# Kernel optimization log

Measured on AMD Instinct MI355X. Metric: run time of the kernel, lower is better.

The kernel has to match this reference:

```python
import jax, jax.numpy as jnp
import numpy as np

NEG_SLOPE = 0.2  # PyG GATConv default negative_slope


def gat_conv(x, src, dst, W, a_src, a_dst, b, n_nodes, concat):
    # x: [N, F_in]; W: [F_in, H*C]; a_src/a_dst: [H, C]; b: [H*C] or [C]
    H, C = a_src.shape
    h = (x @ W).reshape(n_nodes, H, C)                      # [N, H, C]
    al_src = jnp.sum(h * a_src[None], axis=-1)              # [N, H]
    al_dst = jnp.sum(h * a_dst[None], axis=-1)              # [N, H]
    e = jax.nn.leaky_relu(al_src[src] + al_dst[dst], NEG_SLOPE)  # [E, H]
    # segment softmax over incoming edges of each destination node
    m = jax.ops.segment_max(e, dst, num_segments=n_nodes)  # [N, H]
    ex = jnp.exp(e - m[dst])                                # [E, H]
    s = jax.ops.segment_sum(ex, dst, num_segments=n_nodes)  # [N, H]
    alpha = ex / s[dst]                                     # [E, H]
    msg = h[src] * alpha[:, :, None]                        # [E, H, C]
    out = jax.ops.segment_sum(msg, dst, num_segments=n_nodes)  # [N, H, C]
    if concat:
        out = out.reshape(n_nodes, H * C)
    else:
        out = out.mean(axis=1)
    return out + b


def setup_inputs() -> dict:
    key = jax.random.key(0)
    ks = jax.random.split(key, 10)
    N, E = 100000, 800000
    F_in, C1, H, C2 = 128, 32, 8, 16
    x = jax.random.normal(ks[0], (N, F_in), dtype=jnp.float32)
    edge_index = jax.random.randint(ks[1], (2, E), 0, N, dtype=jnp.int64)
    s = 0.05
    return {
        "x": x,
        "edge_index": edge_index,
        "W1": jax.random.normal(ks[2], (F_in, H * C1), dtype=jnp.float32) * s,
        "att_src1": jax.random.normal(ks[3], (H, C1), dtype=jnp.float32) * s,
        "att_dst1": jax.random.normal(ks[4], (H, C1), dtype=jnp.float32) * s,
        "b1": jnp.zeros((H * C1,), dtype=jnp.float32),
        "W2": jax.random.normal(ks[5], (H * C1, H * C2), dtype=jnp.float32) * s,
        "att_src2": jax.random.normal(ks[6], (H, C2), dtype=jnp.float32) * s,
        "att_dst2": jax.random.normal(ks[7], (H, C2), dtype=jnp.float32) * s,
        "b2": jnp.zeros((C2,), dtype=jnp.float32),
    }


def reference(x, edge_index, W1, att_src1, att_dst1, b1, W2, att_src2, att_dst2, b2):
    n = x.shape[0]
    # PyG GATConv default add_self_loops=True (same augmented edge set for both layers)
    loops = jnp.arange(n, dtype=edge_index.dtype)
    src = jnp.concatenate([edge_index[0], loops])
    dst = jnp.concatenate([edge_index[1], loops])
    # dropout_p = 0.0 -> dropout is identity (eval-mode math)
    h = gat_conv(x, src, dst, W1, att_src1, att_dst1, b1, n, concat=True)
    h = jax.nn.elu(h)
    out = gat_conv(h, src, dst, W2, att_src2, att_dst2, b2, n, concat=False)
    return jax.nn.log_softmax(out, axis=-1)
```

## Files before the change

### kernel.cpp

```cpp
#include <hip/hip_runtime.h>
#include <cstdint>
#include <cstddef>


typedef short bf16x8 __attribute__((ext_vector_type(8)));
typedef unsigned short u16x8 __attribute__((ext_vector_type(8)));
typedef float f32x4 __attribute__((ext_vector_type(4)));

__device__ inline unsigned short f2bf(float f) {
  unsigned u = __float_as_uint(f);
  unsigned r = (u + 0x7FFFu + ((u >> 16) & 1u)) >> 16;
  return (unsigned short)r;
}
__device__ inline float bf2f(unsigned short s) {
  return __uint_as_float((unsigned)s << 16);
}

__device__ inline unsigned char fp8enc(float x) {
  unsigned u = __float_as_uint(x);
  unsigned s = u >> 31;
  float ax = fminf(fabsf(x), 448.f);
  unsigned em;
  if (ax >= 0.015625f) {
    unsigned b = __float_as_uint(ax);
    unsigned b2 = b + 0x7FFFFu + ((b >> 20) & 1u);
    em = (b2 >> 20) - 960u;
    if (em > 126u) em = 126u;
  } else {
    em = (unsigned)__float2int_rn(ax * 512.f);
  }
  return (unsigned char)((s << 7) | em);
}
__device__ inline float fp8dec_sw(unsigned b8) {
  unsigned s = b8 >> 7, em = b8 & 0x7Fu;
  float fn = __uint_as_float((s << 31) | ((em + 960u) << 20));
  float fd = (float)em * 0.001953125f;
  fd = s ? -fd : fd;
  return em >= 8u ? fn : fd;
}
__device__ inline void fp8dec4(unsigned w, float* out) {
#if __has_builtin(__builtin_amdgcn_cvt_f32_fp8)
  out[0] = __builtin_amdgcn_cvt_f32_fp8(w, 0);
  out[1] = __builtin_amdgcn_cvt_f32_fp8(w, 1);
  out[2] = __builtin_amdgcn_cvt_f32_fp8(w, 2);
  out[3] = __builtin_amdgcn_cvt_f32_fp8(w, 3);
#else
  out[0] = fp8dec_sw(w & 0xFFu);
  out[1] = fp8dec_sw((w >> 8) & 0xFFu);
  out[2] = fp8dec_sw((w >> 16) & 0xFFu);
  out[3] = fp8dec_sw((w >> 24) & 0xFFu);
#endif
}


__global__ __launch_bounds__(256) void detect_kernel(const int* __restrict__ words,
                                                     int E, int* __restrict__ flag) {
  int t = threadIdx.x;
  int n = E < 1024 ? E : 1024;
  int cnt = 0;
  for (int i = t; i < n; i += 256) cnt += (words[2 * i + 1] != 0) ? 1 : 0;
  for (int m = 1; m < 64; m <<= 1) cnt += __shfl_xor(cnt, m);
  if ((t & 63) == 0 && cnt) atomicAdd(flag, cnt);
}

__global__ __launch_bounds__(256) void extract_kernel(const void* __restrict__ ei,
                                                      int E, int N,
                                                      const int* __restrict__ flag,
                                                      int* __restrict__ src,
                                                      int* __restrict__ dst,
                                                      int* __restrict__ deg) {
  int e = blockIdx.x * 256 + threadIdx.x;
  int ET = E + N;
  if (e >= ET) return;
  int s, d;
  if (e < E) {
    if (flag[0] == 0) {
      const long long* p = (const long long*)ei;
      s = (int)p[e];
      d = (int)p[(size_t)E + e];
    } else {
      const int* p = (const int*)ei;
      s = p[e];
      d = p[E + e];
    }
  } else {
    s = d = e - E;
  }
  src[e] = s;
  dst[e] = d;
  atomicAdd(&deg[d], 1);
}

__global__ __launch_bounds__(256) void scan_a(const int* __restrict__ deg,
                                              int* __restrict__ off,
                                              int* __restrict__ bsum, int N) {
  __shared__ int sh[256];
  int b = blockIdx.x, t = threadIdx.x;
  int base = b * 2048 + t * 8;
  int p[8];
  int run = 0;
#pragma unroll
  for (int j = 0; j < 8; ++j) {
    int v = (base + j < N) ? deg[base + j] : 0;
    run += v;
    p[j] = run;
  }
  sh[t] = run;
  __syncthreads();
  for (int d = 1; d < 256; d <<= 1) {
    int x = (t >= d) ? sh[t - d] : 0;
    __syncthreads();
    if (t >= d) sh[t] += x;
    __syncthreads();
  }
  int excl = sh[t] - run;
#pragma unroll
  for (int j = 0; j < 8; ++j)
    if (base + j < N) off[base + j + 1] = excl + p[j];
  if (t == 255) bsum[b] = sh[255];
}

__global__ void scan_b(int* __restrict__ bsum, int nb) {
  int t = threadIdx.x;
  int orig = (t < nb) ? bsum[t] : 0;
  int v = orig;
  for (int d = 1; d < 64; d <<= 1) {
    int u = __shfl_up(v, d);
    if (t >= d) v += u;
  }
  if (t < nb) bsum[t] = v - orig;
}

__global__ __launch_bounds__(256) void scan_c(int* __restrict__ off,
                                              const int* __restrict__ bsum, int N) {
  int i = blockIdx.x * 256 + threadIdx.x;
  if (i == 0) off[0] = 0;
  if (i >= 1 && i <= N) off[i] += bsum[(i - 1) / 2048];
}

__global__ __launch_bounds__(256) void fill_kernel(const int* __restrict__ src,
                                                   const int* __restrict__ dst,
                                                   const int* __restrict__ off,
                                                   int* __restrict__ deg,
                                                   int* __restrict__ csr, int ET) {
  int e = blockIdx.x * 256 + threadIdx.x;
  if (e >= ET) return;
  int d = dst[e];
  int p = atomicSub(&deg[d], 1) - 1;
  csr[off[d] + p] = src[e];
}

__global__ __launch_bounds__(256) void pack_kernel(const float* __restrict__ W,
                                                   short* __restrict__ Wp,
                                                   int NOUT, int total) {
  int NT = NOUT >> 4;
  for (int idx = blockIdx.x * 256 + threadIdx.x; idx < total;
       idx += gridDim.x * 256) {
    int j = idx & 7;
    int lane = (idx >> 3) & 63;
    int st = idx >> 9;
    int s = st / NT, t = st - s * NT;
    int k = s * 32 + (lane >> 4) * 8 + j;
    int n = t * 16 + (lane & 15);
    Wp[idx] = (short)f2bf(W[(size_t)k * NOUT + n]);
  }
}

template <int K, int NOUT, bool AF32, bool OUT_FP8>
__global__ __launch_bounds__(256) void mfma_gemm(const void* __restrict__ Av,
                                                 const short* __restrict__ Bp,
                                                 short* __restrict__ Cb,
                                                 unsigned char* __restrict__ Cq,
                                                 const float* __restrict__ as,
                                                 const float* __restrict__ ad,
                                                 float* __restrict__ alsO,
                                                 float* __restrict__ aldO, int M) {
  constexpr int KS = K / 32;
  constexpr int NT = NOUT / 16;
  constexpr int RST = NOUT + 8;
  constexpr int QST = NOUT + 16;
  constexpr int C = NOUT / 8;
  __shared__ __align__(16) short lds[64 * RST];
  __shared__ __align__(16) unsigned char ldsq[OUT_FP8 ? 64 * QST : 16];
  const int tid = threadIdx.x;
  const int wave = tid >> 6, lane = tid & 63;
  const int lo = lane & 15, hi = lane >> 4;
  const int rowA = blockIdx.x * 64 + wave * 16 + lo;
  const bool inb = rowA < M;

  f32x4 acc[NT];
#pragma unroll
  for (int t = 0; t < NT; ++t) acc[t] = (f32x4){0.f, 0.f, 0.f, 0.f};

#pragma unroll
  for (int s = 0; s < KS; ++s) {
    bf16x8 af;
    if constexpr (AF32) {
      const float* Ap = (const float*)Av;
      float v[8];
      if (inb) {
        const float4 x0 = *(const float4*)&Ap[(size_t)rowA * K + s * 32 + hi * 8];
        const float4 x1 = *(const float4*)&Ap[(size_t)rowA * K + s * 32 + hi * 8 + 4];
        v[0] = x0.x; v[1] = x0.y; v[2] = x0.z; v[3] = x0.w;
        v[4] = x1.x; v[5] = x1.y; v[6] = x1.z; v[7] = x1.w;
      } else {
#pragma unroll
        for (int j = 0; j < 8; ++j) v[j] = 0.f;
      }
#pragma unroll
      for (int j = 0; j < 8; ++j) af[j] = (short)f2bf(v[j]);
    } else {
      const short* Ab = (const short*)Av;
      if (inb) {
        af = *(const bf16x8*)&Ab[(size_t)rowA * K + s * 32 + hi * 8];
      } else {
#pragma unroll
        for (int j = 0; j < 8; ++j) af[j] = 0;
      }
    }
#pragma unroll
    for (int t = 0; t < NT; ++t) {
      bf16x8 bf = *(const bf16x8*)&Bp[((size_t)(s * NT + t) * 64 + lane) * 8];
      acc[t] = __builtin_amdgcn_mfma_f32_16x16x32_bf16(af, bf, acc[t], 0, 0, 0);
    }
  }

#pragma unroll
  for (int t = 0; t < NT; ++t)
#pragma unroll
    for (int r = 0; r < 4; ++r) {
      int row = wave * 16 + hi * 4 + r;
      lds[row * RST + t * 16 + lo] = (short)f2bf(acc[t][r]);
      if constexpr (OUT_FP8)
        ldsq[row * QST + t * 16 + lo] = fp8enc(acc[t][r]);
    }
  __syncthreads();

  if constexpr (OUT_FP8) {
#pragma unroll
    for (int i = 0; i < (64 * NOUT / 16) / 256; ++i) {
      int v = i * 256 + tid;
      int r = v >> 4;
      int c = v & 15;
      int grow = blockIdx.x * 64 + r;
      if (grow < M)
        *(float4*)&Cq[(size_t)grow * NOUT + c * 16] =
            *(const float4*)&ldsq[r * QST + c * 16];
    }
  } else {
    constexpr int VECS = 64 * NOUT / 8;
#pragma unroll
    for (int i = 0; i < VECS / 256; ++i) {
      int v = i * 256 + tid;
      int r = v / (NOUT / 8);
      int c = v % (NOUT / 8);
      int grow = blockIdx.x * 64 + r;
      if (grow < M)
        *(float4*)&Cb[(size_t)grow * NOUT + c * 8] =
            *(const float4*)&lds[r * RST + c * 8];
    }
  }

  constexpr int SEGS = NOUT / 64;
  if (tid < 64 * SEGS) {
    int r = tid / SEGS, seg = tid % SEGS;
    int grow = blockIdx.x * 64 + r;
    float ps[8], pd[8];
#pragma unroll
    for (int k = 0; k < 8; ++k) { ps[k] = 0.f; pd[k] = 0.f; }
#pragma unroll
    for (int k = 0; k < 8; ++k) {
      int b = seg + SEGS * k;
      u16x8 u = *(const u16x8*)&lds[r * RST + b * 8];
#pragma unroll
      for (int j = 0; j < 8; ++j) {
        float hv = bf2f(u[j]);
        ps[k] = fmaf(hv, as[k * C + seg * 8 + j], ps[k]);
        pd[k] = fmaf(hv, ad[k * C + seg * 8 + j], pd[k]);
      }
    }
#pragma unroll
    for (int d = 1; d < SEGS; d <<= 1)
#pragma unroll
      for (int k = 0; k < 8; ++k) {
        ps[k] += __shfl_xor(ps[k], d);
        pd[k] += __shfl_xor(pd[k], d);
      }
    if (seg == 0 && grow < M) {
      *(float4*)&alsO[(size_t)grow * 8] = make_float4(ps[0], ps[1], ps[2], ps[3]);
      *(float4*)&alsO[(size_t)grow * 8 + 4] = make_float4(ps[4], ps[5], ps[6], ps[7]);
      *(float4*)&aldO[(size_t)grow * 8] = make_float4(pd[0], pd[1], pd[2], pd[3]);
      *(float4*)&aldO[(size_t)grow * 8 + 4] = make_float4(pd[4], pd[5], pd[6], pd[7]);
    }
  }
}

__global__ __launch_bounds__(256) void agg1_kernel(const unsigned char* __restrict__ hq,
                                                   const float* __restrict__ als,
                                                   const float* __restrict__ ald,
                                                   const int* __restrict__ off,
                                                   const int* __restrict__ csr,
                                                   const float* __restrict__ bias,
                                                   short* __restrict__ outb, int N) {
  int wid = blockIdx.x * 4 + (threadIdx.x >> 6);
  if (wid >= N) return;
  int lane = threadIdx.x & 63;
  int rs = off[wid], re = off[wid + 1];
  int es = lane >> 5;
  int gl = lane & 31;
  int head = gl >> 2;
  float aldv = ald[wid * 8 + head];

  float acc[8];
#pragma unroll
  for (int j = 0; j < 8; ++j) acc[j] = 0.f;
  float ws = 0.f;

  int i = rs + es;
  for (; i + 2 < re; i += 4) {
    int s0 = csr[i], s1 = csr[i + 2];
    float e0 = als[s0 * 8 + head] + aldv;
    float e1 = als[s1 * 8 + head] + aldv;
    uint2 u0 = *(const uint2*)&hq[(size_t)s0 * 256 + gl * 8];
    uint2 u1 = *(const uint2*)&hq[(size_t)s1 * 256 + gl * 8];
    e0 = e0 > 0.f ? e0 : 0.2f * e0;
    e1 = e1 > 0.f ? e1 : 0.2f * e1;
    float w0 = __expf(e0), w1 = __expf(e1);
    ws += w0 + w1;
    float d0a[4], d0b[4], d1a[4], d1b[4];
    fp8dec4(u0.x, d0a); fp8dec4(u0.y, d0b);
    fp8dec4(u1.x, d1a); fp8dec4(u1.y, d1b);
#pragma unroll
    for (int j = 0; j < 4; ++j) {
      acc[j] = fmaf(w0, d0a[j], acc[j]);
      acc[j + 4] = fmaf(w0, d0b[j], acc[j + 4]);
      acc[j] = fmaf(w1, d1a[j], acc[j]);
      acc[j + 4] = fmaf(w1, d1b[j], acc[j + 4]);
    }
  }
  if (i < re) {
    int s0 = csr[i];
    float e0 = als[s0 * 8 + head] + aldv;
    uint2 u0 = *(const uint2*)&hq[(size_t)s0 * 256 + gl * 8];
    e0 = e0 > 0.f ? e0 : 0.2f * e0;
    float w0 = __expf(e0);
    ws += w0;
    float d0a[4], d0b[4];
    fp8dec4(u0.x, d0a); fp8dec4(u0.y, d0b);
#pragma unroll
    for (int j = 0; j < 4; ++j) {
      acc[j] = fmaf(w0, d0a[j], acc[j]);
      acc[j + 4] = fmaf(w0, d0b[j], acc[j + 4]);
    }
  }

  ws += __shfl_xor(ws, 32);
#pragma unroll
  for (int j = 0; j < 8; ++j) acc[j] += __shfl_xor(acc[j], 32);
  float inv = 1.f / ws;

  if (lane < 32) {
    u16x8 o;
#pragma unroll
    for (int j = 0; j < 8; ++j) {
      float v = acc[j] * inv + bias[gl * 8 + j];
      o[j] = f2bf(v > 0.f ? v : expm1f(v));
    }
    *(u16x8*)&outb[(size_t)wid * 256 + gl * 8] = o;
  }
}

__global__ __launch_bounds__(256) void agg2_kernel(const short* __restrict__ hb,
                                                   const float* __restrict__ als,
                                                   const float* __restrict__ ald,
                                                   const int* __restrict__ off,
                                                   const int* __restrict__ csr,
                                                   const float* __restrict__ bias,
                                                   float* __restrict__ out, int N) {
  constexpr int LPG = 16;
  constexpr int NS = 4;
  int wid = blockIdx.x * 4 + (threadIdx.x >> 6);
  if (wid >= N) return;
  int lane = threadIdx.x & 63;
  int rs = off[wid], re = off[wid + 1];
  int es = lane / LPG;
  int gl = lane & (LPG - 1);
  int head = gl >> 1;
  float aldv = ald[wid * 8 + head];

  float acc[8];
#pragma unroll
  for (int j = 0; j < 8; ++j) acc[j] = 0.f;
  float ws = 0.f;

  int i = rs + es;
  for (; i + NS < re; i += 2 * NS) {
    int s0 = csr[i], s1 = csr[i + NS];
    float e0 = als[s0 * 8 + head] + aldv;
    float e1 = als[s1 * 8 + head] + aldv;
    u16x8 u0 = *(const u16x8*)&hb[(size_t)s0 * 128 + gl * 8];
    u16x8 u1 = *(const u16x8*)&hb[(size_t)s1 * 128 + gl * 8];
    e0 = e0 > 0.f ? e0 : 0.2f * e0;
    e1 = e1 > 0.f ? e1 : 0.2f * e1;
    float w0 = __expf(e0), w1 = __expf(e1);
    ws += w0 + w1;
#pragma unroll
    for (int j = 0; j < 8; ++j)
      acc[j] = fmaf(w1, bf2f(u1[j]), fmaf(w0, bf2f(u0[j]), acc[j]));
  }
  if (i < re) {
    int s0 = csr[i];
    float e0 = als[s0 * 8 + head] + aldv;
    u16x8 u0 = *(const u16x8*)&hb[(size_t)s0 * 128 + gl * 8];
    e0 = e0 > 0.f ? e0 : 0.2f * e0;
    float w0 = __expf(e0);
    ws += w0;
#pragma unroll
    for (int j = 0; j < 8; ++j) acc[j] = fmaf(w0, bf2f(u0[j]), acc[j]);
  }

#pragma unroll
  for (int d = LPG; d < 64; d <<= 1) {
    ws += __shfl_xor(ws, d);
#pragma unroll
    for (int j = 0; j < 8; ++j) acc[j] += __shfl_xor(acc[j], d);
  }
  float inv = 1.f / ws;

#pragma unroll
  for (int j = 0; j < 8; ++j) acc[j] *= inv;
#pragma unroll
  for (int d = 2; d <= 8; d <<= 1)
#pragma unroll
    for (int j = 0; j < 8; ++j) acc[j] += __shfl_xor(acc[j], d);
  int p = gl & 1;
  float v[8];
#pragma unroll
  for (int j = 0; j < 8; ++j) v[j] = acc[j] * 0.125f + bias[p * 8 + j];
  float m = v[0];
#pragma unroll
  for (int j = 1; j < 8; ++j) m = fmaxf(m, v[j]);
  m = fmaxf(m, __shfl_xor(m, 1));
  float se = 0.f;
#pragma unroll
  for (int j = 0; j < 8; ++j) se += __expf(v[j] - m);
  se += __shfl_xor(se, 1);
  float lse = m + logf(se);
  if (lane < 2) {
    *(float4*)&out[(size_t)wid * 16 + p * 8] =
        make_float4(v[0] - lse, v[1] - lse, v[2] - lse, v[3] - lse);
    *(float4*)&out[(size_t)wid * 16 + p * 8 + 4] =
        make_float4(v[4] - lse, v[5] - lse, v[6] - lse, v[7] - lse);
  }
}


extern "C" void kernel_launch(void* const* d_in, const int* in_sizes, int n_in,
                              void* d_out, int out_size, void* d_ws, size_t ws_size,
                              hipStream_t stream) {
  const float* x = (const float*)d_in[0];
  const void* ei = d_in[1];
  const float* W1 = (const float*)d_in[2];
  const float* as1 = (const float*)d_in[3];
  const float* ad1 = (const float*)d_in[4];
  const float* b1 = (const float*)d_in[5];
  const float* W2 = (const float*)d_in[6];
  const float* as2 = (const float*)d_in[7];
  const float* ad2 = (const float*)d_in[8];
  const float* b2 = (const float*)d_in[9];
  float* out = (float*)d_out;

  const int N = out_size / 16;
  const int E = in_sizes[1] / 2;
  const int ET = E + N;

  char* p = (char*)d_ws;
  auto alloc = [&](size_t bytes) {
    char* r = p;
    p += (bytes + 255) & ~(size_t)255;
    return (void*)r;
  };
  unsigned char* h1q = (unsigned char*)alloc((size_t)N * 256);
  short* hactb = (short*)alloc((size_t)N * 256 * 2);
  short* h2b = (short*)alloc((size_t)N * 128 * 2);
  float* als = (float*)alloc((size_t)N * 8 * 4);
  float* ald = (float*)alloc((size_t)N * 8 * 4);
  int* src32 = (int*)alloc((size_t)ET * 4);
  int* dst32 = (int*)alloc((size_t)ET * 4);
  int* csr = (int*)alloc((size_t)ET * 4);
  int* deg = (int*)alloc((size_t)N * 4);
  int* off = (int*)alloc((size_t)(N + 1) * 4);
  int* bsum = (int*)alloc(256 * 4);
  int* flag = (int*)alloc(256);
  short* W1p = (short*)alloc(128 * 256 * 2);
  short* W2p = (short*)alloc(256 * 128 * 2);

  hipMemsetAsync(deg, 0, (size_t)N * 4, stream);
  hipMemsetAsync(flag, 0, 4, stream);

  detect_kernel<<<1, 256, 0, stream>>>((const int*)ei, E, flag);
  int gridET = (ET + 255) / 256;
  extract_kernel<<<gridET, 256, 0, stream>>>(ei, E, N, flag, src32, dst32, deg);
  int nscan = (N + 2047) / 2048;
  scan_a<<<nscan, 256, 0, stream>>>(deg, off, bsum, N);
  scan_b<<<1, 64, 0, stream>>>(bsum, nscan);
  scan_c<<<(N + 256) / 256, 256, 0, stream>>>(off, bsum, N);
  fill_kernel<<<gridET, 256, 0, stream>>>(src32, dst32, off, deg, csr, ET);

  pack_kernel<<<128, 256, 0, stream>>>(W1, W1p, 256, 128 * 256);
  pack_kernel<<<128, 256, 0, stream>>>(W2, W2p, 128, 256 * 128);

  int gemmGrid = (N + 63) / 64;
  int nodeGrid = (N + 3) / 4;

  mfma_gemm<128, 256, true, true><<<gemmGrid, 256, 0, stream>>>(
      x, W1p, nullptr, h1q, as1, ad1, als, ald, N);
  agg1_kernel<<<nodeGrid, 256, 0, stream>>>(h1q, als, ald, off, csr, b1, hactb, N);
  mfma_gemm<256, 128, false, false><<<gemmGrid, 256, 0, stream>>>(
      hactb, W2p, h2b, nullptr, as2, ad2, als, ald, N);
  agg2_kernel<<<nodeGrid, 256, 0, stream>>>(h2b, als, ald, off, csr, b2, out, N);
}
```

Measured before the change: 338.5 us.

## Fuse edge extraction into layer-1 GEMM, merge scans/packs, use FP8 for layer-2 features

Edge extraction and degree counting are merged into the layer-1 GEMM launch as extra blocks, the two weight-pack kernels become one, and scan_b is folded into scan_c. The two memsets become one. Layer-2 features are now stored as FP8 (reusing the h1q buffer) instead of bf16, halving gather bytes in agg2. Leaky ReLU uses fmaxf. The aim is fewer launches and less memory traffic, at the cost of FP8 precision loss in the second layer and a larger LDS footprint for the second GEMM.

```diff
diff --git a/kernel.cpp b/kernel.cpp
--- a/kernel.cpp
+++ b/kernel.cpp
@@ -63,34 +63,6 @@
   if ((t & 63) == 0 && cnt) atomicAdd(flag, cnt);
 }
 
-__global__ __launch_bounds__(256) void extract_kernel(const void* __restrict__ ei,
-                                                      int E, int N,
-                                                      const int* __restrict__ flag,
-                                                      int* __restrict__ src,
-                                                      int* __restrict__ dst,
-                                                      int* __restrict__ deg) {
-  int e = blockIdx.x * 256 + threadIdx.x;
-  int ET = E + N;
-  if (e >= ET) return;
-  int s, d;
-  if (e < E) {
-    if (flag[0] == 0) {
-      const long long* p = (const long long*)ei;
-      s = (int)p[e];
-      d = (int)p[(size_t)E + e];
-    } else {
-      const int* p = (const int*)ei;
-      s = p[e];
-      d = p[E + e];
-    }
-  } else {
-    s = d = e - E;
-  }
-  src[e] = s;
-  dst[e] = d;
-  atomicAdd(&deg[d], 1);
-}
-
 __global__ __launch_bounds__(256) void scan_a(const int* __restrict__ deg,
                                               int* __restrict__ off,
                                               int* __restrict__ bsum, int N) {
@@ -120,22 +92,27 @@
   if (t == 255) bsum[b] = sh[255];
 }
 
-__global__ void scan_b(int* __restrict__ bsum, int nb) {
+__global__ __launch_bounds__(256) void scan_c(int* __restrict__ off,
+                                              const int* __restrict__ bsum,
+                                              int N, int nb) {
+  __shared__ int sb[64];
   int t = threadIdx.x;
-  int orig = (t < nb) ? bsum[t] : 0;
-  int v = orig;
-  for (int d = 1; d < 64; d <<= 1) {
-    int u = __shfl_up(v, d);
-    if (t >= d) v += u;
-  }
-  if (t < nb) bsum[t] = v - orig;
-}
-
-__global__ __launch_bounds__(256) void scan_c(int* __restrict__ off,
-                                              const int* __restrict__ bsum, int N) {
-  int i = blockIdx.x * 256 + threadIdx.x;
+  if (t < 64) {
+    int v = (t < nb) ? bsum[t] : 0;
+    for (int d = 1; d < 64; d <<= 1) {
+      int u = __shfl_up(v, d);
+      if (t >= d) v += u;
+    }
+    sb[t] = v;
+  }
+  __syncthreads();
+  int i = blockIdx.x * 256 + t;
   if (i == 0) off[0] = 0;
-  if (i >= 1 && i <= N) off[i] += bsum[(i - 1) / 2048];
+  if (i >= 1 && i <= N) {
+    int c = (i - 1) / 2048;
+    int excl = (c == 0) ? 0 : sb[c - 1];
+    off[i] += excl;
+  }
 }
 
 __global__ __launch_bounds__(256) void fill_kernel(const int* __restrict__ src,
@@ -150,42 +127,46 @@
   csr[off[d] + p] = src[e];
 }
 
-__global__ __launch_bounds__(256) void pack_kernel(const float* __restrict__ W,
-                                                   short* __restrict__ Wp,
-                                                   int NOUT, int total) {
+__device__ inline void pack_one(const float* __restrict__ W,
+                                short* __restrict__ Wp, int NOUT, int idx) {
   int NT = NOUT >> 4;
-  for (int idx = blockIdx.x * 256 + threadIdx.x; idx < total;
-       idx += gridDim.x * 256) {
-    int j = idx & 7;
-    int lane = (idx >> 3) & 63;
-    int st = idx >> 9;
-    int s = st / NT, t = st - s * NT;
-    int k = s * 32 + (lane >> 4) * 8 + j;
-    int n = t * 16 + (lane & 15);
-    Wp[idx] = (short)f2bf(W[(size_t)k * NOUT + n]);
-  }
-}
-
-template <int K, int NOUT, bool AF32, bool OUT_FP8>
-__global__ __launch_bounds__(256) void mfma_gemm(const void* __restrict__ Av,
-                                                 const short* __restrict__ Bp,
-                                                 short* __restrict__ Cb,
-                                                 unsigned char* __restrict__ Cq,
-                                                 const float* __restrict__ as,
-                                                 const float* __restrict__ ad,
-                                                 float* __restrict__ alsO,
-                                                 float* __restrict__ aldO, int M) {
+  int j = idx & 7;
+  int lane = (idx >> 3) & 63;
+  int st = idx >> 9;
+  int s = st / NT, t = st - s * NT;
+  int k = s * 32 + (lane >> 4) * 8 + j;
+  int n = t * 16 + (lane & 15);
+  Wp[idx] = (short)f2bf(W[(size_t)k * NOUT + n]);
+}
+
+__global__ __launch_bounds__(256) void pack2_kernel(const float* __restrict__ W1,
+                                                    short* __restrict__ W1p,
+                                                    const float* __restrict__ W2,
+                                                    short* __restrict__ W2p) {
+  int b = blockIdx.x, t = threadIdx.x;
+  if (b < 128) pack_one(W1, W1p, 256, b * 256 + t);
+  else         pack_one(W2, W2p, 128, (b - 128) * 256 + t);
+}
+
+template <int K, int NOUT, bool AF32>
+__device__ void gemm_body(int bx, const void* __restrict__ Av,
+                          const short* __restrict__ Bp,
+                          unsigned char* __restrict__ Cq,
+                          const float* __restrict__ as,
+                          const float* __restrict__ ad,
+                          float* __restrict__ alsO,
+                          float* __restrict__ aldO, int M) {
   constexpr int KS = K / 32;
   constexpr int NT = NOUT / 16;
   constexpr int RST = NOUT + 8;
   constexpr int QST = NOUT + 16;
   constexpr int C = NOUT / 8;
   __shared__ __align__(16) short lds[64 * RST];
-  __shared__ __align__(16) unsigned char ldsq[OUT_FP8 ? 64 * QST : 16];
+  __shared__ __align__(16) unsigned char ldsq[64 * QST];
   const int tid = threadIdx.x;
   const int wave = tid >> 6, lane = tid & 63;
   const int lo = lane & 15, hi = lane >> 4;
-  const int rowA = blockIdx.x * 64 + wave * 16 + lo;
+  const int rowA = bx * 64 + wave * 16 + lo;
   const bool inb = rowA < M;
 
   f32x4 acc[NT];
@@ -231,40 +212,26 @@
     for (int r = 0; r < 4; ++r) {
       int row = wave * 16 + hi * 4 + r;
       lds[row * RST + t * 16 + lo] = (short)f2bf(acc[t][r]);
-      if constexpr (OUT_FP8)
-        ldsq[row * QST + t * 16 + lo] = fp8enc(acc[t][r]);
+      ldsq[row * QST + t * 16 + lo] = fp8enc(acc[t][r]);
     }
   __syncthreads();
 
-  if constexpr (OUT_FP8) {
-#pragma unroll
-    for (int i = 0; i < (64 * NOUT / 16) / 256; ++i) {
-      int v = i * 256 + tid;
-      int r = v >> 4;
-      int c = v & 15;
-      int grow = blockIdx.x * 64 + r;
-      if (grow < M)
-        *(float4*)&Cq[(size_t)grow * NOUT + c * 16] =
-            *(const float4*)&ldsq[r * QST + c * 16];
-    }
-  } else {
-    constexpr int VECS = 64 * NOUT / 8;
-#pragma unroll
-    for (int i = 0; i < VECS / 256; ++i) {
-      int v = i * 256 + tid;
-      int r = v / (NOUT / 8);
-      int c = v % (NOUT / 8);
-      int grow = blockIdx.x * 64 + r;
-      if (grow < M)
-        *(float4*)&Cb[(size_t)grow * NOUT + c * 8] =
-            *(const float4*)&lds[r * RST + c * 8];
-    }
+  constexpr int CPR = NOUT / 16;
+#pragma unroll
+  for (int i = 0; i < (64 * CPR) / 256; ++i) {
+    int v = i * 256 + tid;
+    int r = v / CPR;
+    int c = v % CPR;
+    int grow = bx * 64 + r;
+    if (grow < M)
+      *(float4*)&Cq[(size_t)grow * NOUT + c * 16] =
+          *(const float4*)&ldsq[r * QST + c * 16];
   }
 
   constexpr int SEGS = NOUT / 64;
   if (tid < 64 * SEGS) {
     int r = tid / SEGS, seg = tid % SEGS;
-    int grow = blockIdx.x * 64 + r;
+    int grow = bx * 64 + r;
     float ps[8], pd[8];
 #pragma unroll
     for (int k = 0; k < 8; ++k) { ps[k] = 0.f; pd[k] = 0.f; }
@@ -293,6 +260,51 @@
       *(float4*)&aldO[(size_t)grow * 8 + 4] = make_float4(pd[4], pd[5], pd[6], pd[7]);
     }
   }
+}
+
+__global__ __launch_bounds__(256) void mega1_kernel(
+    const float* __restrict__ x, const short* __restrict__ W1p,
+    unsigned char* __restrict__ h1q, const float* __restrict__ as1,
+    const float* __restrict__ ad1, float* __restrict__ als,
+    float* __restrict__ ald, int M, int gemmGrid,
+    const void* __restrict__ ei, int E, int N, const int* __restrict__ flag,
+    int* __restrict__ src, int* __restrict__ dst, int* __restrict__ deg) {
+  int bx = blockIdx.x;
+  if (bx < gemmGrid) {
+    gemm_body<128, 256, true>(bx, x, W1p, h1q, as1, ad1, als, ald, M);
+  } else {
+    int e = (bx - gemmGrid) * 256 + threadIdx.x;
+    int ET = E + N;
+    if (e >= ET) return;
+    int s, d;
+    if (e < E) {
+      if (flag[0] == 0) {
+        const long long* p = (const long long*)ei;
+        s = (int)p[e];
+        d = (int)p[(size_t)E + e];
+      } else {
+        const int* p = (const int*)ei;
+        s = p[e];
+        d = p[E + e];
+      }
+    } else {
+      s = d = e - E;
+    }
+    src[e] = s;
+    dst[e] = d;
+    atomicAdd(&deg[d], 1);
+  }
+}
+
+template <int K, int NOUT, bool AF32>
+__global__ __launch_bounds__(256) void mfma_gemm(const void* __restrict__ Av,
+                                                 const short* __restrict__ Bp,
+                                                 unsigned char* __restrict__ Cq,
+                                                 const float* __restrict__ as,
+                                                 const float* __restrict__ ad,
+                                                 float* __restrict__ alsO,
+                                                 float* __restrict__ aldO, int M) {
+  gemm_body<K, NOUT, AF32>(blockIdx.x, Av, Bp, Cq, as, ad, alsO, aldO, M);
 }
 
 __global__ __launch_bounds__(256) void agg1_kernel(const unsigned char* __restrict__ hq,
@@ -323,8 +335,8 @@
     float e1 = als[s1 * 8 + head] + aldv;
     uint2 u0 = *(const uint2*)&hq[(size_t)s0 * 256 + gl * 8];
     uint2 u1 = *(const uint2*)&hq[(size_t)s1 * 256 + gl * 8];
-    e0 = e0 > 0.f ? e0 : 0.2f * e0;
-    e1 = e1 > 0.f ? e1 : 0.2f * e1;
+    e0 = fmaxf(e0, 0.2f * e0);
+    e1 = fmaxf(e1, 0.2f * e1);
     float w0 = __expf(e0), w1 = __expf(e1);
     ws += w0 + w1;
     float d0a[4], d0b[4], d1a[4], d1b[4];
@@ -342,7 +354,7 @@
     int s0 = csr[i];
     float e0 = als[s0 * 8 + head] + aldv;
     uint2 u0 = *(const uint2*)&hq[(size_t)s0 * 256 + gl * 8];
-    e0 = e0 > 0.f ? e0 : 0.2f * e0;
+    e0 = fmaxf(e0, 0.2f * e0);
     float w0 = __expf(e0);
     ws += w0;
     float d0a[4], d0b[4];
@@ -370,21 +382,19 @@
   }
 }
 
-__global__ __launch_bounds__(256) void agg2_kernel(const short* __restrict__ hb,
+__global__ __launch_bounds__(256) void agg2_kernel(const unsigned char* __restrict__ hq,
                                                    const float* __restrict__ als,
                                                    const float* __restrict__ ald,
                                                    const int* __restrict__ off,
                                                    const int* __restrict__ csr,
                                                    const float* __restrict__ bias,
                                                    float* __restrict__ out, int N) {
-  constexpr int LPG = 16;
-  constexpr int NS = 4;
   int wid = blockIdx.x * 4 + (threadIdx.x >> 6);
   if (wid >= N) return;
   int lane = threadIdx.x & 63;
   int rs = off[wid], re = off[wid + 1];
-  int es = lane / LPG;
-  int gl = lane & (LPG - 1);
+  int es = lane >> 4;
+  int gl = lane & 15;
   int head = gl >> 1;
   float aldv = ald[wid * 8 + head];
 
@@ -394,33 +404,38 @@
   float ws = 0.f;
 
   int i = rs + es;
-  for (; i + NS < re; i += 2 * NS) {
-    int s0 = csr[i], s1 = csr[i + NS];
+  for (; i + 4 < re; i += 8) {
+    int s0 = csr[i], s1 = csr[i + 4];
     float e0 = als[s0 * 8 + head] + aldv;
     float e1 = als[s1 * 8 + head] + aldv;
-    u16x8 u0 = *(const u16x8*)&hb[(size_t)s0 * 128 + gl * 8];
-    u16x8 u1 = *(const u16x8*)&hb[(size_t)s1 * 128 + gl * 8];
-    e0 = e0 > 0.f ? e0 : 0.2f * e0;
-    e1 = e1 > 0.f ? e1 : 0.2f * e1;
+    uint2 u0 = *(const uint2*)&hq[(size_t)s0 * 128 + gl * 8];
+    uint2 u1 = *(const uint2*)&hq[(size_t)s1 * 128 + gl * 8];
+    e0 = fmaxf(e0, 0.2f * e0);
+    e1 = fmaxf(e1, 0.2f * e1);
     float w0 = __expf(e0), w1 = __expf(e1);
     ws += w0 + w1;
+    float d0[8], d1[8];
+    fp8dec4(u0.x, d0); fp8dec4(u0.y, d0 + 4);
+    fp8dec4(u1.x, d1); fp8dec4(u1.y, d1 + 4);
 #pragma unroll
     for (int j = 0; j < 8; ++j)
-      acc[j] = fmaf(w1, bf2f(u1[j]), fmaf(w0, bf2f(u0[j]), acc[j]));
+      acc[j] = fmaf(w1, d1[j], fmaf(w0, d0[j], acc[j]));
   }
   if (i < re) {
     int s0 = csr[i];
     float e0 = als[s0 * 8 + head] + aldv;
-    u16x8 u0 = *(const u16x8*)&hb[(size_t)s0 * 128 + gl * 8];
-    e0 = e0 > 0.f ? e0 : 0.2f * e0;
+    uint2 u0 = *(const uint2*)&hq[(size_t)s0 * 128 + gl * 8];
+    e0 = fmaxf(e0, 0.2f * e0);
     float w0 = __expf(e0);
     ws += w0;
-#pragma unroll
-    for (int j = 0; j < 8; ++j) acc[j] = fmaf(w0, bf2f(u0[j]), acc[j]);
-  }
-
-#pragma unroll
-  for (int d = LPG; d < 64; d <<= 1) {
+    float d0[8];
+    fp8dec4(u0.x, d0); fp8dec4(u0.y, d0 + 4);
+#pragma unroll
+    for (int j = 0; j < 8; ++j) acc[j] = fmaf(w0, d0[j], acc[j]);
+  }
+
+#pragma unroll
+  for (int d = 16; d < 64; d <<= 1) {
     ws += __shfl_xor(ws, d);
 #pragma unroll
     for (int j = 0; j < 8; ++j) acc[j] += __shfl_xor(acc[j], d);
@@ -482,41 +497,38 @@
   };
   unsigned char* h1q = (unsigned char*)alloc((size_t)N * 256);
   short* hactb = (short*)alloc((size_t)N * 256 * 2);
-  short* h2b = (short*)alloc((size_t)N * 128 * 2);
   float* als = (float*)alloc((size_t)N * 8 * 4);
   float* ald = (float*)alloc((size_t)N * 8 * 4);
   int* src32 = (int*)alloc((size_t)ET * 4);
   int* dst32 = (int*)alloc((size_t)ET * 4);
   int* csr = (int*)alloc((size_t)ET * 4);
   int* deg = (int*)alloc((size_t)N * 4);
+  int* flag = (int*)alloc(256);
   int* off = (int*)alloc((size_t)(N + 1) * 4);
   int* bsum = (int*)alloc(256 * 4);
-  int* flag = (int*)alloc(256);
   short* W1p = (short*)alloc(128 * 256 * 2);
   short* W2p = (short*)alloc(256 * 128 * 2);
-
-  hipMemsetAsync(deg, 0, (size_t)N * 4, stream);
-  hipMemsetAsync(flag, 0, 4, stream);
+  unsigned char* h2q = h1q;
+
+  hipMemsetAsync(deg, 0, (((size_t)N * 4 + 255) & ~(size_t)255) + 4, stream);
 
   detect_kernel<<<1, 256, 0, stream>>>((const int*)ei, E, flag);
+  pack2_kernel<<<256, 256, 0, stream>>>(W1, W1p, W2, W2p);
+
+  int gemmGrid = (N + 63) / 64;
   int gridET = (ET + 255) / 256;
-  extract_kernel<<<gridET, 256, 0, stream>>>(ei, E, N, flag, src32, dst32, deg);
+  int nodeGrid = (N + 3) / 4;
   int nscan = (N + 2047) / 2048;
+
+  mega1_kernel<<<gemmGrid + gridET, 256, 0, stream>>>(
+      x, W1p, h1q, as1, ad1, als, ald, N, gemmGrid, ei, E, N, flag, src32,
+      dst32, deg);
   scan_a<<<nscan, 256, 0, stream>>>(deg, off, bsum, N);
-  scan_b<<<1, 64, 0, stream>>>(bsum, nscan);
-  scan_c<<<(N + 256) / 256, 256, 0, stream>>>(off, bsum, N);
+  scan_c<<<(N + 256) / 256, 256, 0, stream>>>(off, bsum, N, nscan);
   fill_kernel<<<gridET, 256, 0, stream>>>(src32, dst32, off, deg, csr, ET);
 
-  pack_kernel<<<128, 256, 0, stream>>>(W1, W1p, 256, 128 * 256);
-  pack_kernel<<<128, 256, 0, stream>>>(W2, W2p, 128, 256 * 128);
-
-  int gemmGrid = (N + 63) / 64;
-  int nodeGrid = (N + 3) / 4;
-
-  mfma_gemm<128, 256, true, true><<<gemmGrid, 256, 0, stream>>>(
-      x, W1p, nullptr, h1q, as1, ad1, als, ald, N);
   agg1_kernel<<<nodeGrid, 256, 0, stream>>>(h1q, als, ald, off, csr, b1, hactb, N);
-  mfma_gemm<256, 128, false, false><<<gemmGrid, 256, 0, stream>>>(
-      hactb, W2p, h2b, nullptr, as2, ad2, als, ald, N);
-  agg2_kernel<<<nodeGrid, 256, 0, stream>>>(h2b, als, ald, off, csr, b2, out, N);
-}
+  mfma_gemm<256, 128, false><<<gemmGrid, 256, 0, stream>>>(
+      hactb, W2p, h2q, as2, ad2, als, ald, N);
+  agg2_kernel<<<nodeGrid, 256, 0, stream>>>(h2q, als, ald, off, csr, b2, out, N);
+}
```

New measurement: 324.6 us. 1.04x faster.
